# Kernel optimization log

Hardware: AMD Instinct MI355X
Metric: run time of the kernel (lower is better)

Reference implementation:

```python
import jax, jax.numpy as jnp
import numpy as np

B, N, F, H = 8, 256, 512, 256  # batch, nodes (=hidden_dim), feature_dim, hidden_dim


def _pair_scores(x, y, W1a, W1b, b1, W2, b2):
    """sigmoid(MLP(concat(x_i, y_j))) for all pairs, without materializing concat.

    x, y: [B, N, H]. W1a/W1b are the two halves of the Linear(2H -> H) weight.
    Returns [B, N, N].
    """
    a = jnp.einsum('bnh,hk->bnk', x, W1a)          # contribution of row i
    c = jnp.einsum('bnh,hk->bnk', y, W1b)          # contribution of row j
    h = jax.nn.relu(a[:, :, None, :] + c[:, None, :, :] + b1)  # [B,N,N,H]
    s = jnp.einsum('bijh,h->bij', h, W2) + b2
    return jax.nn.sigmoid(s)


def setup_inputs() -> dict:
    key = jax.random.key(0)
    ks = jax.random.split(key, 16)
    sc = 0.02
    return {
        'image_features': jax.random.normal(ks[0], (B, N, F), jnp.float32),
        'text_features': jax.random.normal(ks[1], (B, N, F), jnp.float32),
        # feature_transform: Linear(F->H), ReLU, Linear(H->H)
        'ft_W1': jax.random.normal(ks[2], (F, H), jnp.float32) * sc,
        'ft_b1': jnp.zeros((H,), jnp.float32),
        'ft_W2': jax.random.normal(ks[3], (H, H), jnp.float32) * sc,
        'ft_b2': jnp.zeros((H,), jnp.float32),
        # structure_learning: Linear(2H->H) split into two H x H halves, Linear(H->1)
        'sl_W1a': jax.random.normal(ks[4], (H, H), jnp.float32) * sc,
        'sl_W1b': jax.random.normal(ks[5], (H, H), jnp.float32) * sc,
        'sl_b1': jnp.zeros((H,), jnp.float32),
        'sl_W2': jax.random.normal(ks[6], (H,), jnp.float32) * sc,
        'sl_b2': jnp.zeros((), jnp.float32),
        # causal_net: Linear(2H->H) split, Linear(H->1)
        'cn_W1a': jax.random.normal(ks[7], (H, H), jnp.float32) * sc,
        'cn_W1b': jax.random.normal(ks[8], (H, H), jnp.float32) * sc,
        'cn_b1': jnp.zeros((H,), jnp.float32),
        'cn_W2': jax.random.normal(ks[9], (H,), jnp.float32) * sc,
        'cn_b2': jnp.zeros((), jnp.float32),
    }


def reference(image_features, text_features,
              ft_W1, ft_b1, ft_W2, ft_b2,
              sl_W1a, sl_W1b, sl_b1, sl_W2, sl_b2,
              cn_W1a, cn_W1b, cn_b1, cn_W2, cn_b2):
    # --- StructuralLearning ---
    def feat(x):
        h = jax.nn.relu(jnp.einsum('bnf,fh->bnh', x, ft_W1) + ft_b1)
        return jnp.einsum('bnh,hk->bnk', h, ft_W2) + ft_b2

    img_h = feat(image_features)   # [B,N,H]
    txt_h = feat(text_features)    # [B,N,H]
    structure = _pair_scores(img_h, txt_h, sl_W1a, sl_W1b, sl_b1, sl_W2, sl_b2)  # [B,N,N]

    # --- CausalDiscovery (batched over all node pairs; sigmoid(structure) > 0
    # everywhere so every (i,j) is an edge). DAG cycle removal is a CPU-side
    # networkx post-process and is omitted from the differentiable reference. ---
    causal_matrix = _pair_scores(structure, structure, cn_W1a, cn_W1b, cn_b1, cn_W2, cn_b2)

    # --- verify_causal_invariance ---
    stability = jnp.mean(jnp.abs(causal_matrix - jnp.roll(causal_matrix, 1, axis=0)))
    consistency = jnp.mean(jnp.std(causal_matrix, axis=0, ddof=1))  # torch.std is unbiased
    invariance_score = 1.0 - (stability + consistency) / 2

    return structure, causal_matrix, invariance_score
```

## Files before the change

### kernel.cpp

```cpp
#include <hip/hip_runtime.h>
#include <math.h>

#define B_ 8
#define N_ 256
#define F_ 512
#define H_ 256

typedef __attribute__((ext_vector_type(8))) short short8;
typedef __attribute__((ext_vector_type(4))) float floatx4;
typedef _Float16 h2 __attribute__((ext_vector_type(2)));

__device__ __forceinline__ unsigned int f2bf_bits(float f) {
    unsigned int u = __float_as_uint(f);
    return (u + 0x7fffu + ((u >> 16) & 1u)) >> 16;
}
__device__ __forceinline__ unsigned int pack2bf(float a, float b) {
    return f2bf_bits(a) | (f2bf_bits(b) << 16);
}
__device__ __forceinline__ h2 as_h2(unsigned int u) {
    union { unsigned int u; h2 h; } x; x.u = u; return x.h;
}
__device__ __forceinline__ h2 relu2(h2 t) {
    h2 z; z.x = (_Float16)0; z.y = (_Float16)0;
#if __has_builtin(__builtin_elementwise_max)
    return __builtin_elementwise_max(t, z);
#else
    t.x = t.x > z.x ? t.x : z.x;
    t.y = t.y > z.y ? t.y : z.y;
    return t;
#endif
}

__global__ __launch_bounds__(256) void prep_weights(
    const float* __restrict__ ftW1, const float* __restrict__ ftW2,
    const float* __restrict__ slW1a, const float* __restrict__ slW1b,
    const float* __restrict__ cnW1a, const float* __restrict__ cnW1b,
    const float* __restrict__ ftb2, const float* __restrict__ slb1,
    unsigned short* __restrict__ wt, float* __restrict__ bA, float* __restrict__ bB)
{
    if (blockIdx.x >= 224) {
        const int second = (blockIdx.x == 225);
        const float* W = second ? slW1b : slW1a;
        const int n = threadIdx.x;
        float s0 = 0.f, s1 = 0.f, s2 = 0.f, s3 = 0.f;
#pragma unroll 4
        for (int k = 0; k < 256; k += 4) {
            s0 = fmaf(ftb2[k],     W[(k)     * 256 + n], s0);
            s1 = fmaf(ftb2[k + 1], W[(k + 1) * 256 + n], s1);
            s2 = fmaf(ftb2[k + 2], W[(k + 2) * 256 + n], s2);
            s3 = fmaf(ftb2[k + 3], W[(k + 3) * 256 + n], s3);
        }
        float s = (s0 + s1) + (s2 + s3);
        if (second) bB[n] = s + slb1[n];
        else        bA[n] = s;
        return;
    }

    int t = blockIdx.x * 256 + threadIdx.x;
    if (t < 49152) {
        const float* src; int K; unsigned short* dst;
        if (t < 16384) { src = ftW1; K = 512; dst = wt; }
        else {
            int m  = (t - 16384) >> 13;
            t = (t - 16384) & 8191; K = 256;
            switch (m) {
                case 0:  src = slW1a; dst = wt + 131072; break;
                case 1:  src = slW1b; dst = wt + 196608; break;
                case 2:  src = cnW1a; dst = wt + 262144; break;
                default: src = cnW1b; dst = wt + 327680; break;
            }
        }
        const int n  = t & 255;
        const int k0 = (t >> 8) * 8;
        unsigned int p[4];
#pragma unroll
        for (int j = 0; j < 4; ++j) {
            float f0 = src[(size_t)(k0 + 2 * j)     * 256 + n];
            float f1 = src[(size_t)(k0 + 2 * j + 1) * 256 + n];
            p[j] = pack2bf(f0, f1);
        }
        *(uint4*)(dst + (size_t)n * K + k0) = make_uint4(p[0], p[1], p[2], p[3]);
    } else {
        const int lt = t - 49152;
        const int k  = lt >> 5;
        const int n0 = (lt & 31) * 8;
        const float* src = ftW2 + (size_t)k * 256 + n0;
        float4 f0 = *(const float4*)(src);
        float4 f1 = *(const float4*)(src + 4);
        unsigned short* dst = wt + 393216 + (size_t)k * 256 + n0;
        *(uint4*)dst = make_uint4(pack2bf(f0.x, f0.y), pack2bf(f0.z, f0.w),
                                  pack2bf(f1.x, f1.y), pack2bf(f1.z, f1.w));
    }
}

struct GJob {
    const void* A0; const void* A1; int aSplitBlk; int aBf16;
    const unsigned short* Wt0; const unsigned short* Wt1;
    const float* bias0; const float* bias1;
    int wRowSplitBlk; int wColSplitBlk;
    void* out; int outMode; int ldOut; int K; int relu;
};

__global__ __launch_bounds__(256) void gemm_mfma(GJob j0, GJob j1, int j0By)
{
    __shared__ unsigned short As[2][64][40];
    __shared__ unsigned short Bs[2][64][40];

    const bool firstJob = ((int)blockIdx.y < j0By);
    const GJob j = firstJob ? j0 : j1;
    const int by = firstJob ? blockIdx.y : blockIdx.y - j0By;
    const int bx = blockIdx.x;
    const int tid = threadIdx.x;
    const int K = j.K;

    const void* Abase; int arow0;
    if (by < j.aSplitBlk) { Abase = j.A0; arow0 = by * 64; }
    else                  { Abase = j.A1; arow0 = (by - j.aSplitBlk) * 64; }

    int wcolBlk = bx;
    bool second;
    if (j.wColSplitBlk > 0) {
        second = (bx >= j.wColSplitBlk);
        if (second) wcolBlk = bx - j.wColSplitBlk;
    } else {
        second = (by >= j.wRowSplitBlk);
    }
    const unsigned short* Wt = second ? j.Wt1 : j.Wt0;
    const float* bias        = second ? j.bias1 : j.bias0;
    const int wcol = wcolBlk * 64;

    const int r    = tid >> 2;
    const int kq   = (tid & 3) * 8;
    const int lane = tid & 63;
    const int wv   = tid >> 6;
    const int col  = lane & 15;
    const int quad = lane >> 4;

    floatx4 acc[4] = {};

    uint4 apack, bpack;
    float4 af0, af1;
    const unsigned short* Abf = (const unsigned short*)Abase + (size_t)(arow0 + r) * K + kq;
    const float*          Afp = (const float*)Abase + (size_t)(arow0 + r) * K + kq;
    const unsigned short* Wp  = Wt + (size_t)(wcol + r) * K + kq;

    if (j.aBf16) apack = *(const uint4*)(Abf);
    else { af0 = *(const float4*)(Afp); af1 = *(const float4*)(Afp + 4); }
    bpack = *(const uint4*)(Wp);

    int p = 0;
    for (int k0 = 0; k0 < K; k0 += 32) {
        uint4 aw;
        if (j.aBf16) aw = apack;
        else aw = make_uint4(pack2bf(af0.x, af0.y), pack2bf(af0.z, af0.w),
                             pack2bf(af1.x, af1.y), pack2bf(af1.z, af1.w));
        uint4 bw = bpack;

        *(uint4*)&As[p][r][kq] = aw;
        *(uint4*)&Bs[p][r][kq] = bw;

        if (k0 + 32 < K) {
            if (j.aBf16) apack = *(const uint4*)(Abf + k0 + 32);
            else {
                af0 = *(const float4*)(Afp + k0 + 32);
                af1 = *(const float4*)(Afp + k0 + 32 + 4);
            }
            bpack = *(const uint4*)(Wp + k0 + 32);
        }

        __syncthreads();

        short8 bfrag = *(const short8*)&Bs[p][wv * 16 + col][quad * 8];
#pragma unroll
        for (int tm = 0; tm < 4; ++tm) {
            short8 afrag = *(const short8*)&As[p][tm * 16 + col][quad * 8];
            acc[tm] = __builtin_amdgcn_mfma_f32_16x16x32_bf16(afrag, bfrag, acc[tm], 0, 0, 0);
        }
        p ^= 1;
    }

    const int ocol = bx * 64 + wv * 16 + col;
    const int bcol = wcol + wv * 16 + col;
    const float bv = bias ? bias[bcol] : 0.f;
#pragma unroll
    for (int tm = 0; tm < 4; ++tm) {
#pragma unroll
        for (int rr = 0; rr < 4; ++rr) {
            float v = acc[tm][rr] + bv;
            if (j.relu) v = fmaxf(v, 0.f);
            const size_t o = (size_t)(by * 64 + tm * 16 + quad * 4 + rr) * j.ldOut + ocol;
            if (j.outMode == 0)      ((float*)j.out)[o] = v;
            else if (j.outMode == 1) ((unsigned short*)j.out)[o] = (unsigned short)f2bf_bits(v);
            else                     ((_Float16*)j.out)[o] = (_Float16)v;
        }
    }
}

__global__ __launch_bounds__(256) void pair_score(
    const unsigned short* __restrict__ Abase, int ldA,
    const unsigned short* __restrict__ Cbase, int ldC,
    const float* __restrict__ W2, const float* __restrict__ b2p,
    float* __restrict__ out)
{
    __shared__ unsigned short aS[64][256];
    __shared__ unsigned short cS[32][256];

    const int tid = threadIdx.x;
    const int b   = blockIdx.z;
    const int i0b = blockIdx.y * 64;
    const int j0b = blockIdx.x * 32;

    {
        const int rr = tid >> 3;
        const int c8 = tid & 7;
#pragma unroll
        for (int rep = 0; rep < 8; ++rep) {
            const int li = rr + 32 * (rep & 1);
            const int ch = c8 + 8 * (rep >> 1);
            uint4 v = *(const uint4*)(Abase + ((size_t)b * N_ + i0b + li) * ldA + ch * 8);
            *(uint4*)&aS[li][(ch ^ ((li >> 1) & 7)) * 8] = v;
        }
#pragma unroll
        for (int rep = 0; rep < 4; ++rep) {
            const int ch = c8 + 8 * rep;
            uint4 v = *(const uint4*)(Cbase + ((size_t)b * N_ + j0b + rr) * ldC + ch * 8);
            *(uint4*)&cS[rr][(ch ^ ((rr >> 1) & 7)) * 8] = v;
        }
    }
    __syncthreads();

    const int ti = tid >> 4, tj = tid & 15;
    const int ia = ti * 4, jc = tj * 2;
    const int k01 = (2 * ti) & 7;
    const int k23 = (2 * ti + 1) & 7;
    const int kc  = tj & 7;

    float s[4][2] = {};

#pragma unroll 4
    for (int ch = 0; ch < 32; ++ch) {
        const uint4 a0 = *(const uint4*)&aS[ia    ][(ch ^ k01) * 8];
        const uint4 a1 = *(const uint4*)&aS[ia + 1][(ch ^ k01) * 8];
        const uint4 a2 = *(const uint4*)&aS[ia + 2][(ch ^ k23) * 8];
        const uint4 a3 = *(const uint4*)&aS[ia + 3][(ch ^ k23) * 8];
        const uint4 c0 = *(const uint4*)&cS[jc    ][(ch ^ kc) * 8];
        const uint4 c1 = *(const uint4*)&cS[jc + 1][(ch ^ kc) * 8];
        const float* w = &W2[ch * 8];
#pragma unroll
        for (int u = 0; u < 4; ++u) {
            const float w0 = w[2 * u], w1 = w[2 * u + 1];
            const h2 hc0 = as_h2(((const unsigned int*)&c0)[u]);
            const h2 hc1 = as_h2(((const unsigned int*)&c1)[u]);
#define ACC2(su, ha, hc) { h2 t_ = relu2((ha) + (hc)); \
    su = fmaf((float)t_.x, w0, su); su = fmaf((float)t_.y, w1, su); }
            {
                const h2 ha = as_h2(((const unsigned int*)&a0)[u]);
                ACC2(s[0][0], ha, hc0); ACC2(s[0][1], ha, hc1);
            }
            {
                const h2 ha = as_h2(((const unsigned int*)&a1)[u]);
                ACC2(s[1][0], ha, hc0); ACC2(s[1][1], ha, hc1);
            }
            {
                const h2 ha = as_h2(((const unsigned int*)&a2)[u]);
                ACC2(s[2][0], ha, hc0); ACC2(s[2][1], ha, hc1);
            }
            {
                const h2 ha = as_h2(((const unsigned int*)&a3)[u]);
                ACC2(s[3][0], ha, hc0); ACC2(s[3][1], ha, hc1);
            }
#undef ACC2
        }
    }

    const float bb = b2p[0];
#pragma unroll
    for (int rr = 0; rr < 4; ++rr) {
        float2 o;
        o.x = 1.f / (1.f + expf(-(s[rr][0] + bb)));
        o.y = 1.f / (1.f + expf(-(s[rr][1] + bb)));
        *(float2*)&out[((size_t)b * N_ + i0b + ia + rr) * N_ + j0b + jc] = o;
    }
}

__global__ __launch_bounds__(256) void invariance_partial(
    const float* __restrict__ causal, float* __restrict__ accum,
    float* __restrict__ out_scalar)
{
    const int idx = blockIdx.x * 256 + threadIdx.x;
    float x[B_];
#pragma unroll
    for (int b = 0; b < B_; ++b) x[b] = causal[(size_t)b * (N_ * N_) + idx];

    float stab = 0.f, mean = 0.f;
#pragma unroll
    for (int b = 0; b < B_; ++b) {
        stab += fabsf(x[b] - x[(b + B_ - 1) % B_]);
        mean += x[b];
    }
    mean *= (1.f / B_);
    float var = 0.f;
#pragma unroll
    for (int b = 0; b < B_; ++b) {
        float d = x[b] - mean;
        var = fmaf(d, d, var);
    }
    float sd = sqrtf(var * (1.f / (B_ - 1)));

#pragma unroll
    for (int off = 32; off > 0; off >>= 1) {
        stab += __shfl_down(stab, off, 64);
        sd   += __shfl_down(sd, off, 64);
    }

    __shared__ float red[8];
    if ((threadIdx.x & 63) == 0) {
        red[threadIdx.x >> 6]       = stab;
        red[4 + (threadIdx.x >> 6)] = sd;
    }
    __syncthreads();
    if (threadIdx.x == 0) {
        float s = (red[0] + red[1]) + (red[2] + red[3]);
        float d = (red[4] + red[5]) + (red[6] + red[7]);
        atomicAdd(&accum[0], s);
        atomicAdd(&accum[1], d);
        __threadfence();
        unsigned int prev = atomicAdd((unsigned int*)&accum[2], 1u);
        if (prev == 255u) {
            float st  = atomicAdd(&accum[0], 0.f);
            float sdt = atomicAdd(&accum[1], 0.f);
            float stability   = st  * (1.f / (float)(B_ * N_ * N_));
            float consistency = sdt * (1.f / (float)(N_ * N_));
            out_scalar[0] = 1.f - (stability + consistency) * 0.5f;
        }
    }
}

extern "C" void kernel_launch(void* const* d_in, const int* in_sizes, int n_in,
                              void* d_out, int out_size, void* d_ws, size_t ws_size,
                              hipStream_t stream)
{
    const float* img   = (const float*)d_in[0];
    const float* txt   = (const float*)d_in[1];
    const float* ftW1  = (const float*)d_in[2];
    const float* ftb1  = (const float*)d_in[3];
    const float* ftW2  = (const float*)d_in[4];
    const float* ftb2  = (const float*)d_in[5];
    const float* slW1a = (const float*)d_in[6];
    const float* slW1b = (const float*)d_in[7];
    const float* slb1  = (const float*)d_in[8];
    const float* slW2  = (const float*)d_in[9];
    const float* slb2  = (const float*)d_in[10];
    const float* cnW1a = (const float*)d_in[11];
    const float* cnW1b = (const float*)d_in[12];
    const float* cnb1  = (const float*)d_in[13];
    const float* cnW2  = (const float*)d_in[14];
    const float* cnb2  = (const float*)d_in[15];

    float* out       = (float*)d_out;
    float* structure = out;
    float* causal    = out + (size_t)B_ * N_ * N_;
    float* inv       = out + 2 * (size_t)B_ * N_ * N_;

    unsigned short* wt     = (unsigned short*)d_ws;
    unsigned short* wcombT = wt + 458752;
    float* bA    = (float*)(wt + 589824);
    float* bB    = bA + 256;
    float* accum = bA + 512;
    unsigned short* h1b  = wt + 655360;
    unsigned short* acb  = wt + 1703936;
    unsigned short* ac2b = acb;

    hipMemsetAsync(accum, 0, 4 * sizeof(float), stream);

    dim3 blk(256);
    const int BIG = 1 << 20;

    const unsigned short* wtFT1 = wt;
    const unsigned short* wtSLA = wt + 131072;
    const unsigned short* wtSLB = wt + 196608;
    const unsigned short* wtCNA = wt + 262144;
    const unsigned short* wtCNB = wt + 327680;
    const unsigned short* ftW2r = wt + 393216;

    prep_weights<<<dim3(226), blk, 0, stream>>>(
        ftW1, ftW2, slW1a, slW1b, cnW1a, cnW1b, ftb2, slb1, wt, bA, bB);

    {
        GJob g1  = { img, txt, 32, 0, wtFT1, wtFT1, ftb1, ftb1, BIG, 0,
                     h1b, 1, 256, 512, 1 };
        GJob wcb = { wtSLA, wtSLB, 4, 1, ftW2r, ftW2r, nullptr, nullptr, BIG, 0,
                     wcombT, 1, 256, 256, 0 };
        gemm_mfma<<<dim3(4, 72), blk, 0, stream>>>(g1, wcb, 64);
    }

    {
        GJob g2 = { h1b, h1b, BIG, 1, wcombT, wcombT + 65536, bA, bB, 32, 0,
                    acb, 2, 256, 256, 0 };
        gemm_mfma<<<dim3(4, 64), blk, 0, stream>>>(g2, g2, 64);
    }

    pair_score<<<dim3(8, 4, 8), blk, 0, stream>>>(
        acb, 256, acb + (size_t)2048 * 256, 256, slW2, slb2, structure);

    {
        GJob g4 = { structure, structure, BIG, 0, wtCNA, wtCNB, nullptr, cnb1, BIG, 4,
                    ac2b, 2, 512, 256, 0 };
        gemm_mfma<<<dim3(8, 32), blk, 0, stream>>>(g4, g4, 32);
    }

    pair_score<<<dim3(8, 4, 8), blk, 0, stream>>>(
        ac2b, 512, ac2b + 256, 512, cnW2, cnb2, causal);

    invariance_partial<<<dim3(N_ * N_ / 256), blk, 0, stream>>>(causal, accum, inv);
}
```

Baseline: 166.8 us.

## Fuse all stages into one persistent megakernel with grid barriers

```diff
diff --git a/kernel.cpp b/kernel.cpp
--- a/kernel.cpp
+++ b/kernel.cpp
@@ -5,6 +5,7 @@
 #define N_ 256
 #define F_ 512
 #define H_ 256
+#define NBLK 256
 
 typedef __attribute__((ext_vector_type(8))) short short8;
 typedef __attribute__((ext_vector_type(4))) float floatx4;
@@ -31,15 +32,34 @@
 #endif
 }
 
-__global__ __launch_bounds__(256) void prep_weights(
+union alignas(16) SharedU {
+    struct { unsigned short As[2][64][40]; unsigned short Bs[2][64][40]; } g;
+    struct { unsigned short aS[64][256]; unsigned short cS[32][256]; } p;
+    float red[8];
+};
+
+__device__ __forceinline__ void grid_barrier(unsigned* cnt) {
+    __syncthreads();
+    if (threadIdx.x == 0) {
+        __threadfence();
+        __hip_atomic_fetch_add(cnt, 1u, __ATOMIC_RELEASE, __HIP_MEMORY_SCOPE_AGENT);
+        while (__hip_atomic_load(cnt, __ATOMIC_ACQUIRE, __HIP_MEMORY_SCOPE_AGENT) < NBLK)
+            __builtin_amdgcn_s_sleep(2);
+        __threadfence();
+    }
+    __syncthreads();
+}
+
+__device__ void prep_block(
     const float* __restrict__ ftW1, const float* __restrict__ ftW2,
     const float* __restrict__ slW1a, const float* __restrict__ slW1b,
     const float* __restrict__ cnW1a, const float* __restrict__ cnW1b,
     const float* __restrict__ ftb2, const float* __restrict__ slb1,
-    unsigned short* __restrict__ wt, float* __restrict__ bA, float* __restrict__ bB)
-{
-    if (blockIdx.x >= 224) {
-        const int second = (blockIdx.x == 225);
+    unsigned short* __restrict__ wt, float* __restrict__ bA, float* __restrict__ bB,
+    int blk)
+{
+    if (blk >= 224) {
+        const int second = (blk == 225);
         const float* W = second ? slW1b : slW1a;
         const int n = threadIdx.x;
         float s0 = 0.f, s1 = 0.f, s2 = 0.f, s3 = 0.f;
@@ -56,7 +76,7 @@
         return;
     }
 
-    int t = blockIdx.x * 256 + threadIdx.x;
+    int t = blk * 256 + threadIdx.x;
     if (t < 49152) {
         const float* src; int K; unsigned short* dst;
         if (t < 16384) { src = ftW1; K = 512; dst = wt; }
@@ -101,15 +121,8 @@
     void* out; int outMode; int ldOut; int K; int relu;
 };
 
-__global__ __launch_bounds__(256) void gemm_mfma(GJob j0, GJob j1, int j0By)
-{
-    __shared__ unsigned short As[2][64][40];
-    __shared__ unsigned short Bs[2][64][40];
-
-    const bool firstJob = ((int)blockIdx.y < j0By);
-    const GJob j = firstJob ? j0 : j1;
-    const int by = firstJob ? blockIdx.y : blockIdx.y - j0By;
-    const int bx = blockIdx.x;
+__device__ void gemm_tile(const GJob& j, int bx, int by, SharedU& sh)
+{
     const int tid = threadIdx.x;
     const int K = j.K;
 
@@ -156,8 +169,8 @@
                              pack2bf(af1.x, af1.y), pack2bf(af1.z, af1.w));
         uint4 bw = bpack;
 
-        *(uint4*)&As[p][r][kq] = aw;
-        *(uint4*)&Bs[p][r][kq] = bw;
+        *(uint4*)&sh.g.As[p][r][kq] = aw;
+        *(uint4*)&sh.g.Bs[p][r][kq] = bw;
 
         if (k0 + 32 < K) {
             if (j.aBf16) apack = *(const uint4*)(Abf + k0 + 32);
@@ -170,10 +183,10 @@
 
         __syncthreads();
 
-        short8 bfrag = *(const short8*)&Bs[p][wv * 16 + col][quad * 8];
+        short8 bfrag = *(const short8*)&sh.g.Bs[p][wv * 16 + col][quad * 8];
 #pragma unroll
         for (int tm = 0; tm < 4; ++tm) {
-            short8 afrag = *(const short8*)&As[p][tm * 16 + col][quad * 8];
+            short8 afrag = *(const short8*)&sh.g.As[p][tm * 16 + col][quad * 8];
             acc[tm] = __builtin_amdgcn_mfma_f32_16x16x32_bf16(afrag, bfrag, acc[tm], 0, 0, 0);
         }
         p ^= 1;
@@ -196,19 +209,16 @@
     }
 }
 
-__global__ __launch_bounds__(256) void pair_score(
+__device__ void pair_tile(
     const unsigned short* __restrict__ Abase, int ldA,
     const unsigned short* __restrict__ Cbase, int ldC,
     const float* __restrict__ W2, const float* __restrict__ b2p,
-    float* __restrict__ out)
-{
-    __shared__ unsigned short aS[64][256];
-    __shared__ unsigned short cS[32][256];
-
+    float* __restrict__ out, int bx, int by, int bz, SharedU& sh)
+{
     const int tid = threadIdx.x;
-    const int b   = blockIdx.z;
-    const int i0b = blockIdx.y * 64;
-    const int j0b = blockIdx.x * 32;
+    const int b   = bz;
+    const int i0b = by * 64;
+    const int j0b = bx * 32;
 
     {
         const int rr = tid >> 3;
@@ -218,13 +228,13 @@
             const int li = rr + 32 * (rep & 1);
             const int ch = c8 + 8 * (rep >> 1);
             uint4 v = *(const uint4*)(Abase + ((size_t)b * N_ + i0b + li) * ldA + ch * 8);
-            *(uint4*)&aS[li][(ch ^ ((li >> 1) & 7)) * 8] = v;
+            *(uint4*)&sh.p.aS[li][(ch ^ ((li >> 1) & 7)) * 8] = v;
         }
 #pragma unroll
         for (int rep = 0; rep < 4; ++rep) {
             const int ch = c8 + 8 * rep;
             uint4 v = *(const uint4*)(Cbase + ((size_t)b * N_ + j0b + rr) * ldC + ch * 8);
-            *(uint4*)&cS[rr][(ch ^ ((rr >> 1) & 7)) * 8] = v;
+            *(uint4*)&sh.p.cS[rr][(ch ^ ((rr >> 1) & 7)) * 8] = v;
         }
     }
     __syncthreads();
@@ -239,12 +249,12 @@
 
 #pragma unroll 4
     for (int ch = 0; ch < 32; ++ch) {
-        const uint4 a0 = *(const uint4*)&aS[ia    ][(ch ^ k01) * 8];
-        const uint4 a1 = *(const uint4*)&aS[ia + 1][(ch ^ k01) * 8];
-        const uint4 a2 = *(const uint4*)&aS[ia + 2][(ch ^ k23) * 8];
-        const uint4 a3 = *(const uint4*)&aS[ia + 3][(ch ^ k23) * 8];
-        const uint4 c0 = *(const uint4*)&cS[jc    ][(ch ^ kc) * 8];
-        const uint4 c1 = *(const uint4*)&cS[jc + 1][(ch ^ kc) * 8];
+        const uint4 a0 = *(const uint4*)&sh.p.aS[ia    ][(ch ^ k01) * 8];
+        const uint4 a1 = *(const uint4*)&sh.p.aS[ia + 1][(ch ^ k01) * 8];
+        const uint4 a2 = *(const uint4*)&sh.p.aS[ia + 2][(ch ^ k23) * 8];
+        const uint4 a3 = *(const uint4*)&sh.p.aS[ia + 3][(ch ^ k23) * 8];
+        const uint4 c0 = *(const uint4*)&sh.p.cS[jc    ][(ch ^ kc) * 8];
+        const uint4 c1 = *(const uint4*)&sh.p.cS[jc + 1][(ch ^ kc) * 8];
         const float* w = &W2[ch * 8];
 #pragma unroll
         for (int u = 0; u < 4; ++u) {
@@ -283,11 +293,11 @@
     }
 }
 
-__global__ __launch_bounds__(256) void invariance_partial(
+__device__ void inv_block(
     const float* __restrict__ causal, float* __restrict__ accum,
-    float* __restrict__ out_scalar)
-{
-    const int idx = blockIdx.x * 256 + threadIdx.x;
+    float* __restrict__ out_scalar, int blk, SharedU& sh)
+{
+    const int idx = blk * 256 + threadIdx.x;
     float x[B_];
 #pragma unroll
     for (int b = 0; b < B_; ++b) x[b] = causal[(size_t)b * (N_ * N_) + idx];
@@ -313,15 +323,14 @@
         sd   += __shfl_down(sd, off, 64);
     }
 
-    __shared__ float red[8];
     if ((threadIdx.x & 63) == 0) {
-        red[threadIdx.x >> 6]       = stab;
-        red[4 + (threadIdx.x >> 6)] = sd;
+        sh.red[threadIdx.x >> 6]       = stab;
+        sh.red[4 + (threadIdx.x >> 6)] = sd;
     }
     __syncthreads();
     if (threadIdx.x == 0) {
-        float s = (red[0] + red[1]) + (red[2] + red[3]);
-        float d = (red[4] + red[5]) + (red[6] + red[7]);
+        float s = (sh.red[0] + sh.red[1]) + (sh.red[2] + sh.red[3]);
+        float d = (sh.red[4] + sh.red[5]) + (sh.red[6] + sh.red[7]);
         atomicAdd(&accum[0], s);
         atomicAdd(&accum[1], d);
         __threadfence();
@@ -336,81 +345,103 @@
     }
 }
 
+struct MegaP {
+    const float *img, *txt, *ftW1, *ftb1, *ftW2, *ftb2;
+    const float *slW1a, *slW1b, *slb1, *slW2, *slb2;
+    const float *cnW1a, *cnW1b, *cnb1, *cnW2, *cnb2;
+    unsigned short *wt, *wcombT, *h1b, *acb;
+    float *bA, *bB, *accum;
+    unsigned *bar;
+    float *structure, *causal, *invOut;
+};
+
+__global__ __launch_bounds__(256) void mega(MegaP P)
+{
+    __shared__ SharedU sh;
+    const int blk = blockIdx.x;
+    const int BIG = 1 << 20;
+
+    if (blk < 226)
+        prep_block(P.ftW1, P.ftW2, P.slW1a, P.slW1b, P.cnW1a, P.cnW1b,
+                   P.ftb2, P.slb1, P.wt, P.bA, P.bB, blk);
+    grid_barrier(&P.bar[0]);
+
+    const unsigned short* wtFT1 = P.wt;
+    const unsigned short* wtSLA = P.wt + 131072;
+    const unsigned short* wtSLB = P.wt + 196608;
+    const unsigned short* wtCNA = P.wt + 262144;
+    const unsigned short* wtCNB = P.wt + 327680;
+    const unsigned short* ftW2r = P.wt + 393216;
+
+    {
+        GJob g1 = { P.img, P.txt, 32, 0, wtFT1, wtFT1, P.ftb1, P.ftb1, BIG, 0,
+                    P.h1b, 1, 256, 512, 1 };
+        gemm_tile(g1, blk & 3, blk >> 2, sh);
+        if (blk < 32) {
+            __syncthreads();
+            GJob wcb = { wtSLA, wtSLB, 4, 1, ftW2r, ftW2r, nullptr, nullptr, BIG, 0,
+                         P.wcombT, 1, 256, 256, 0 };
+            gemm_tile(wcb, blk & 3, blk >> 2, sh);
+        }
+    }
+    grid_barrier(&P.bar[1]);
+
+    {
+        GJob g2 = { P.h1b, P.h1b, BIG, 1, P.wcombT, P.wcombT + 65536, P.bA, P.bB,
+                    32, 0, P.acb, 2, 256, 256, 0 };
+        gemm_tile(g2, blk & 3, blk >> 2, sh);
+    }
+    grid_barrier(&P.bar[2]);
+
+    pair_tile(P.acb, 256, P.acb + (size_t)2048 * 256, 256, P.slW2, P.slb2,
+              P.structure, blk & 7, (blk >> 3) & 3, blk >> 5, sh);
+    grid_barrier(&P.bar[3]);
+
+    {
+        GJob g4 = { P.structure, P.structure, BIG, 0, wtCNA, wtCNB, nullptr, P.cnb1,
+                    BIG, 4, P.acb, 2, 512, 256, 0 };
+        gemm_tile(g4, blk & 7, blk >> 3, sh);
+    }
+    grid_barrier(&P.bar[4]);
+
+    pair_tile(P.acb, 512, P.acb + 256, 512, P.cnW2, P.cnb2,
+              P.causal, blk & 7, (blk >> 3) & 3, blk >> 5, sh);
+    grid_barrier(&P.bar[5]);
+
+    inv_block(P.causal, P.accum, P.invOut, blk, sh);
+}
+
 extern "C" void kernel_launch(void* const* d_in, const int* in_sizes, int n_in,
                               void* d_out, int out_size, void* d_ws, size_t ws_size,
                               hipStream_t stream)
 {
-    const float* img   = (const float*)d_in[0];
-    const float* txt   = (const float*)d_in[1];
-    const float* ftW1  = (const float*)d_in[2];
-    const float* ftb1  = (const float*)d_in[3];
-    const float* ftW2  = (const float*)d_in[4];
-    const float* ftb2  = (const float*)d_in[5];
-    const float* slW1a = (const float*)d_in[6];
-    const float* slW1b = (const float*)d_in[7];
-    const float* slb1  = (const float*)d_in[8];
-    const float* slW2  = (const float*)d_in[9];
-    const float* slb2  = (const float*)d_in[10];
-    const float* cnW1a = (const float*)d_in[11];
-    const float* cnW1b = (const float*)d_in[12];
-    const float* cnb1  = (const float*)d_in[13];
-    const float* cnW2  = (const float*)d_in[14];
-    const float* cnb2  = (const float*)d_in[15];
-
-    float* out       = (float*)d_out;
-    float* structure = out;
-    float* causal    = out + (size_t)B_ * N_ * N_;
-    float* inv       = out + 2 * (size_t)B_ * N_ * N_;
+    float* out = (float*)d_out;
 
     unsigned short* wt     = (unsigned short*)d_ws;
     unsigned short* wcombT = wt + 458752;
-    float* bA    = (float*)(wt + 589824);
-    float* bB    = bA + 256;
-    float* accum = bA + 512;
-    unsigned short* h1b  = wt + 655360;
-    unsigned short* acb  = wt + 1703936;
-    unsigned short* ac2b = acb;
-
-    hipMemsetAsync(accum, 0, 4 * sizeof(float), stream);
-
-    dim3 blk(256);
-    const int BIG = 1 << 20;
-
-    const unsigned short* wtFT1 = wt;
-    const unsigned short* wtSLA = wt + 131072;
-    const unsigned short* wtSLB = wt + 196608;
-    const unsigned short* wtCNA = wt + 262144;
-    const unsigned short* wtCNB = wt + 327680;
-    const unsigned short* ftW2r = wt + 393216;
-
-    prep_weights<<<dim3(226), blk, 0, stream>>>(
-        ftW1, ftW2, slW1a, slW1b, cnW1a, cnW1b, ftb2, slb1, wt, bA, bB);
-
-    {
-        GJob g1  = { img, txt, 32, 0, wtFT1, wtFT1, ftb1, ftb1, BIG, 0,
-                     h1b, 1, 256, 512, 1 };
-        GJob wcb = { wtSLA, wtSLB, 4, 1, ftW2r, ftW2r, nullptr, nullptr, BIG, 0,
-                     wcombT, 1, 256, 256, 0 };
-        gemm_mfma<<<dim3(4, 72), blk, 0, stream>>>(g1, wcb, 64);
-    }
-
-    {
-        GJob g2 = { h1b, h1b, BIG, 1, wcombT, wcombT + 65536, bA, bB, 32, 0,
-                    acb, 2, 256, 256, 0 };
-        gemm_mfma<<<dim3(4, 64), blk, 0, stream>>>(g2, g2, 64);
-    }
-
-    pair_score<<<dim3(8, 4, 8), blk, 0, stream>>>(
-        acb, 256, acb + (size_t)2048 * 256, 256, slW2, slb2, structure);
-
-    {
-        GJob g4 = { structure, structure, BIG, 0, wtCNA, wtCNB, nullptr, cnb1, BIG, 4,
-                    ac2b, 2, 512, 256, 0 };
-        gemm_mfma<<<dim3(8, 32), blk, 0, stream>>>(g4, g4, 32);
-    }
-
-    pair_score<<<dim3(8, 4, 8), blk, 0, stream>>>(
-        ac2b, 512, ac2b + 256, 512, cnW2, cnb2, causal);
-
-    invariance_partial<<<dim3(N_ * N_ / 256), blk, 0, stream>>>(causal, accum, inv);
-}
+    unsigned* bar   = (unsigned*)(wt + 589824);
+    float*    accum = (float*)(bar + 8);
+    float*    bA    = (float*)(wt + 589888);
+    float*    bB    = bA + 256;
+    unsigned short* h1b = wt + 655360;
+    unsigned short* acb = wt + 1703936;
+
+    hipMemsetAsync(bar, 0, 48, stream);
+
+    MegaP P;
+    P.img = (const float*)d_in[0];  P.txt = (const float*)d_in[1];
+    P.ftW1 = (const float*)d_in[2]; P.ftb1 = (const float*)d_in[3];
+    P.ftW2 = (const float*)d_in[4]; P.ftb2 = (const float*)d_in[5];
+    P.slW1a = (const float*)d_in[6]; P.slW1b = (const float*)d_in[7];
+    P.slb1 = (const float*)d_in[8];  P.slW2 = (const float*)d_in[9];
+    P.slb2 = (const float*)d_in[10]; P.cnW1a = (const float*)d_in[11];
+    P.cnW1b = (const float*)d_in[12]; P.cnb1 = (const float*)d_in[13];
+    P.cnW2 = (const float*)d_in[14]; P.cnb2 = (const float*)d_in[15];
+    P.wt = wt; P.wcombT = wcombT; P.h1b = h1b; P.acb = acb;
+    P.bA = bA; P.bB = bB; P.accum = accum; P.bar = bar;
+    P.structure = out;
+    P.causal    = out + (size_t)B_ * N_ * N_;
+    P.invOut    = out + 2 * (size_t)B_ * N_ * N_;
+
+    mega<<<dim3(NBLK), dim3(256), 0, stream>>>(P);
+}
```

Result: slower. 345.0 us (+106.9%).
